# Performance work log

Hardware: AMD Instinct MI355X
Metric: run time of the kernel (lower is better)

The kernel has to match this reference:

```python
import jax, jax.numpy as jnp
import numpy as np


def _sobel_weights():
    # ImageGradientsLayer: fixed Sobel x/y filters, shape (O=2, I=1, 3, 3)
    gx = jnp.array([[-1., 0., 1.], [-2., 0., 2.], [-1., 0., 1.]], dtype=jnp.float32)
    gy = jnp.array([[-1., -2., -1.], [0., 0., 0.], [1., 2., 1.]], dtype=jnp.float32)
    return jnp.stack([gx, gy])[:, None, :, :]


def _orientation_weights():
    # SIFTOrientationLayer: 8 unit orientation vectors + 2x2 identity, shape (10, 2)
    ratios = jnp.arange(0.125, 2.125, 0.25, dtype=jnp.float32)  # 8 values
    ang = ratios * jnp.pi
    vec = jnp.stack([jnp.cos(ang), jnp.sin(ang)], axis=1)  # (8, 2)
    return jnp.concatenate([vec, jnp.eye(2, dtype=jnp.float32)], axis=0)  # (10, 2)


def setup_inputs() -> dict:
    key = jax.random.key(0)
    x = jax.random.normal(key, (8, 1, 1024, 1024), dtype=jnp.float32)
    return {"x": x, "sobel_w": _sobel_weights(), "orient_w": _orientation_weights()}


def reference(x, sobel_w, orient_w):
    # 1) ImageGradientsLayer: 3x3 Sobel conv, padding=1 -> (B, 2, H, W)
    grads = jax.lax.conv_general_dilated(
        x, sobel_w, window_strides=(1, 1), padding=((1, 1), (1, 1)),
        dimension_numbers=("NCHW", "OIHW", "NCHW"))
    # 2) SIFTOrientationLayer: 1x1 conv == channel projection -> (B, 10, H, W)
    proj = jnp.einsum("bchw,oc->bohw", grads, orient_w)
    # 3) HistogramLayer: one-hot(argmax of orientation dots) * gradient magnitude
    cosines = proj[:, :8]          # (B, 8, H, W)
    im_grads = proj[:, 8:]         # (B, 2, H, W) == grads (identity rows)
    magnitudes = jnp.sqrt(jnp.sum(im_grads * im_grads, axis=1))  # (B, H, W)
    max_idx = jnp.argmax(cosines, axis=1)                        # (B, H, W)
    onehot = jax.nn.one_hot(max_idx, 8, axis=1, dtype=x.dtype)   # (B, 8, H, W)
    hist = onehot * magnitudes[:, None, :, :]
    # 4) SubGridAccumulationLayer: depthwise 4x4 all-ones conv, pad 2 -> (B, 8, H+1, W+1)
    ones_k = jnp.ones((8, 1, 4, 4), dtype=x.dtype)
    out = jax.lax.conv_general_dilated(
        hist, ones_k, window_strides=(1, 1), padding=((2, 2), (2, 2)),
        dimension_numbers=("NCHW", "OIHW", "NCHW"), feature_group_count=8)
    return out
```

## Files before the change

kernel.cpp:

```cpp
#include <hip/hip_runtime.h>
#include <math.h>


#define WPB 4
#define TWC 61
#define WTH 16
#define BTH (WPB*WTH)
#define XC 66
#define XR (BTH+5)

__global__ __launch_bounds__(256, 4)
void sift_fused(const float* __restrict__ x,
                const float* __restrict__ ow,
                float* __restrict__ out)
{
    __shared__ float sx[XR * XC];

    const int tid  = threadIdx.x;
    const int lane = tid & 63;
    const int wv   = tid >> 6;
    const int j0 = blockIdx.x * TWC;
    const int r0 = blockIdx.y * BTH;
    const int bb = blockIdx.z;

    const float* xb = x + (size_t)bb * 1024 * 1024;
    for (int p = tid; p < XR * XC; p += 256) {
        int r = p / XC, c = p - r * XC;
        int gr = r0 - 3 + r, gc = j0 - 3 + c;
        float v = 0.0f;
        if ((unsigned)gr < 1024u && (unsigned)gc < 1024u)
            v = xb[(size_t)gr * 1024 + gc];
        sx[p] = v;
    }
    __syncthreads();

    float wcn[8], wsn[8];
    #pragma unroll
    for (int o = 0; o < 8; ++o) { wcn[o] = ow[2*o]; wsn[o] = ow[2*o+1]; }

    const int gcol = j0 - 2 + lane;
    const bool colok = (unsigned)gcol < 1024u;
    const int gj = j0 + lane;
    const bool canstore = (lane < TWC) && (gj <= 1024);
    const int rbase = r0 + WTH * wv;
    const int hbase = rbase - 2;
    const float* sxw = sx + (WTH * wv) * XC + lane;
    float* outb = out + (size_t)bb * 8u * 1025u * 1025u + gj;

    float cs0[8], cs1[8], cs2[8], cs3[8];
    #pragma unroll
    for (int o = 0; o < 8; ++o) { cs0[o]=0.f; cs1[o]=0.f; cs2[o]=0.f; cs3[o]=0.f; }

    float a0 = sxw[0],  a1 = sxw[1],    a2 = sxw[2];
    float e0 = sxw[XC], e1 = sxw[XC+1], e2 = sxw[XC+2];

#define HROW(J, D0,CT0, D1,CT1, D2,CT2, D3,CT3) { \
    float n0 = sxw[((J)+2)*XC], n1 = sxw[((J)+2)*XC+1], n2 = sxw[((J)+2)*XC+2]; \
    float gx = (a2 - a0) + 2.0f*(e2 - e0) + (n2 - n0); \
    float gy = (n0 + 2.0f*n1 + n2) - (a0 + 2.0f*a1 + a2); \
    int hrow = hbase + (J); \
    float m = (colok && (unsigned)hrow < 1024u) ? sqrtf(gx*gx + gy*gy) : 0.0f; \
    float best = gx*wcn[0] + gy*wsn[0]; int idx = 0; \
    _Pragma("unroll") \
    for (int o = 1; o < 8; ++o) { \
        float co = gx*wcn[o] + gy*wsn[o]; \
        if (co > best) { best = co; idx = o; } \
    } \
    _Pragma("unroll") \
    for (int o = 0; o < 8; ++o) { \
        float cb = (idx == o) ? m : 0.0f; \
        if (D0) CT0[o] += cb; \
        if (D1) CT1[o] += cb; \
        if (D2) CT2[o] += cb; \
        if (D3) CT3[o] += cb; \
    } \
    a0 = e0; a1 = e1; a2 = e2; e0 = n0; e1 = n1; e2 = n2; \
}

#define FIN(T, CS) { \
    int orow = rbase + (T); \
    bool ok = canstore && (orow <= 1024); \
    _Pragma("unroll") \
    for (int o = 0; o < 8; ++o) { \
        float v = CS[o]; \
        v += __shfl_down(v, 1); \
        v += __shfl_down(v, 2); \
        if (ok) outb[(size_t)o * (1025u*1025u) + (size_t)orow * 1025u] = v; \
        CS[o] = 0.0f; \
    } \
}

#define QUAD(J) \
    HROW((J),   1,cs0, 1,cs3, 1,cs2, 1,cs1) FIN((J)-3, cs1) \
    HROW((J)+1, 1,cs1, 1,cs0, 1,cs3, 1,cs2) FIN((J)-2, cs2) \
    HROW((J)+2, 1,cs2, 1,cs1, 1,cs0, 1,cs3) FIN((J)-1, cs3) \
    HROW((J)+3, 1,cs3, 1,cs2, 1,cs1, 1,cs0) FIN((J),   cs0)

    HROW(0, 1,cs0, 0,cs0, 0,cs0, 0,cs0)
    HROW(1, 1,cs1, 1,cs0, 0,cs0, 0,cs0)
    HROW(2, 1,cs2, 1,cs1, 1,cs0, 0,cs0)
    HROW(3, 1,cs3, 1,cs2, 1,cs1, 1,cs0) FIN(0, cs0)
    QUAD(4) QUAD(8) QUAD(12)
    HROW(16, 0,cs0, 1,cs3, 1,cs2, 1,cs1) FIN(13, cs1)
    HROW(17, 0,cs0, 0,cs0, 1,cs3, 1,cs2) FIN(14, cs2)
    HROW(18, 0,cs0, 0,cs0, 0,cs0, 1,cs3) FIN(15, cs3)

#undef QUAD
#undef FIN
#undef HROW
}

extern "C" void kernel_launch(void* const* d_in, const int* in_sizes, int n_in,
                              void* d_out, int out_size, void* d_ws, size_t ws_size,
                              hipStream_t stream)
{
    const float* x  = (const float*)d_in[0];
    const float* ow = (const float*)d_in[2];
    float* out = (float*)d_out;

    dim3 grid((1025 + TWC - 1) / TWC,
              (1025 + BTH - 1) / BTH,
              8);
    sift_fused<<<grid, 256, 0, stream>>>(x, ow, out);
}
```

Before: 101.8 us.

## Restructure sliding-window accumulation with pairwise partial sums and a rolled loop

The fused Sobel/orientation/histogram/box-sum kernel now keeps the vertical 4-row box sum as pairwise partial sums, (row j + row j+1) combined with an earlier pair, instead of four separate accumulators that each get eight adds per row. It also precomputes per-row horizontal Sobel differences and weighted sums once per loaded row, uses a tree-based argmax, and rolls the main row loop to shrink code size and register pressure. Warps whose rows lie entirely beyond the image exit early, and the occupancy hint is raised from 4 to 5. The risks are a changed instruction schedule from the rolled loop and possible register spills under the tighter launch bound.

```diff
diff --git a/kernel.cpp b/kernel.cpp
--- a/kernel.cpp
+++ b/kernel.cpp
@@ -2,14 +2,15 @@
 #include <math.h>
 
 
-#define WPB 4
 #define TWC 61
 #define WTH 16
+#define WPB 4
 #define BTH (WPB*WTH)
 #define XC 66
 #define XR (BTH+5)
+#define PLANE 1050625
 
-__global__ __launch_bounds__(256, 4)
+__global__ __launch_bounds__(256, 5)
 void sift_fused(const float* __restrict__ x,
                 const float* __restrict__ ow,
                 float* __restrict__ out)
@@ -34,6 +35,9 @@
     }
     __syncthreads();
 
+    const int rbase = r0 + WTH * wv;
+    if (rbase > 1024) return;
+
     float wcn[8], wsn[8];
     #pragma unroll
     for (int o = 0; o < 8; ++o) { wcn[o] = ow[2*o]; wsn[o] = ow[2*o+1]; }
@@ -42,72 +46,83 @@
     const bool colok = (unsigned)gcol < 1024u;
     const int gj = j0 + lane;
     const bool canstore = (lane < TWC) && (gj <= 1024);
-    const int rbase = r0 + WTH * wv;
-    const int hbase = rbase - 2;
-    const float* sxw = sx + (WTH * wv) * XC + lane;
-    float* outb = out + (size_t)bb * 8u * 1025u * 1025u + gj;
 
-    float cs0[8], cs1[8], cs2[8], cs3[8];
+    float* po[8];
     #pragma unroll
-    for (int o = 0; o < 8; ++o) { cs0[o]=0.f; cs1[o]=0.f; cs2[o]=0.f; cs3[o]=0.f; }
+    for (int o = 0; o < 8; ++o) po[o] = out + (size_t)(bb * 8 + o) * PLANE;
 
-    float a0 = sxw[0],  a1 = sxw[1],    a2 = sxw[2];
-    float e0 = sxw[XC], e1 = sxw[XC+1], e2 = sxw[XC+2];
+    const float* px = sx + (WTH * wv) * XC + lane;
+    int hrow = rbase - 2;
+    int orow = rbase;
+    int vo   = rbase * 1025 + gj;
 
-#define HROW(J, D0,CT0, D1,CT1, D2,CT2, D3,CT3) { \
-    float n0 = sxw[((J)+2)*XC], n1 = sxw[((J)+2)*XC+1], n2 = sxw[((J)+2)*XC+2]; \
-    float gx = (a2 - a0) + 2.0f*(e2 - e0) + (n2 - n0); \
-    float gy = (n0 + 2.0f*n1 + n2) - (a0 + 2.0f*a1 + a2); \
-    int hrow = hbase + (J); \
-    float m = (colok && (unsigned)hrow < 1024u) ? sqrtf(gx*gx + gy*gy) : 0.0f; \
-    float best = gx*wcn[0] + gy*wsn[0]; int idx = 0; \
-    _Pragma("unroll") \
-    for (int o = 1; o < 8; ++o) { \
-        float co = gx*wcn[o] + gy*wsn[o]; \
-        if (co > best) { best = co; idx = o; } \
-    } \
-    _Pragma("unroll") \
-    for (int o = 0; o < 8; ++o) { \
-        float cb = (idx == o) ? m : 0.0f; \
-        if (D0) CT0[o] += cb; \
-        if (D1) CT1[o] += cb; \
-        if (D2) CT2[o] += cb; \
-        if (D3) CT3[o] += cb; \
-    } \
-    a0 = e0; a1 = e1; a2 = e2; e0 = n0; e1 = n1; e2 = n2; \
+    float dd0, dd1, dd2, dd3, ww0, ww1, ww2, ww3;
+    float cA[8], cB[8], PP0[8], PP1[8], PP2[8], PP3[8];
+
+#define XROWLOAD(DD, WW) { \
+    float n0 = px[0], n1 = px[1], n2 = px[2]; px += XC; \
+    DD = n2 - n0; \
+    WW = n0 + 2.0f*n1 + n2; \
 }
 
-#define FIN(T, CS) { \
-    int orow = rbase + (T); \
-    bool ok = canstore && (orow <= 1024); \
+#define HSTEP(DT, DM, DB, WT, WB, CP, CC, PR, PC, DOP, DOFIN) { \
+    XROWLOAD(DB, WB) \
+    float gx = DT + 2.0f*DM + DB; \
+    float gy = WB - WT; \
+    float msq = gx*gx + gy*gy; \
+    float m = (colok && (unsigned)hrow < 1024u) \
+                ? __builtin_amdgcn_sqrtf(msq) : 0.0f; \
+    hrow++; \
+    float pj0 = gx*wcn[0] + gy*wsn[0]; \
+    float pj1 = gx*wcn[1] + gy*wsn[1]; \
+    float pj2 = gx*wcn[2] + gy*wsn[2]; \
+    float pj3 = gx*wcn[3] + gy*wsn[3]; \
+    float pj4 = gx*wcn[4] + gy*wsn[4]; \
+    float pj5 = gx*wcn[5] + gy*wsn[5]; \
+    float pj6 = gx*wcn[6] + gy*wsn[6]; \
+    float pj7 = gx*wcn[7] + gy*wsn[7]; \
+    bool g01 = pj1 > pj0; float b01 = g01 ? pj1 : pj0; int i01 = g01 ? 1 : 0; \
+    bool g23 = pj3 > pj2; float b23 = g23 ? pj3 : pj2; int i23 = g23 ? 3 : 2; \
+    bool g45 = pj5 > pj4; float b45 = g45 ? pj5 : pj4; int i45 = g45 ? 5 : 4; \
+    bool g67 = pj7 > pj6; float b67 = g67 ? pj7 : pj6; int i67 = g67 ? 7 : 6; \
+    bool gA = b23 > b01; float bA = gA ? b23 : b01; int iA = gA ? i23 : i01; \
+    bool gB = b67 > b45; float bB = gB ? b67 : b45; int iB = gB ? i67 : i45; \
+    int idx = (bB > bA) ? iB : iA; \
     _Pragma("unroll") \
-    for (int o = 0; o < 8; ++o) { \
-        float v = CS[o]; \
-        v += __shfl_down(v, 1); \
-        v += __shfl_down(v, 2); \
-        if (ok) outb[(size_t)o * (1025u*1025u) + (size_t)orow * 1025u] = v; \
-        CS[o] = 0.0f; \
+    for (int o = 0; o < 8; ++o) CC[o] = (idx == o) ? m : 0.0f; \
+    if (DOP) { \
+        _Pragma("unroll") \
+        for (int o = 0; o < 8; ++o) PC[o] = CP[o] + CC[o]; \
+    } \
+    if (DOFIN) { \
+        bool ok = canstore && (orow <= 1024); \
+        _Pragma("unroll") \
+        for (int o = 0; o < 8; ++o) { \
+            float v = PR[o] + PC[o]; \
+            v += __shfl_down(v, 1); \
+            v += __shfl_down(v, 2); \
+            if (ok) po[o][vo] = v; \
+        } \
+        vo += 1025; orow++; \
     } \
 }
 
-#define QUAD(J) \
-    HROW((J),   1,cs0, 1,cs3, 1,cs2, 1,cs1) FIN((J)-3, cs1) \
-    HROW((J)+1, 1,cs1, 1,cs0, 1,cs3, 1,cs2) FIN((J)-2, cs2) \
-    HROW((J)+2, 1,cs2, 1,cs1, 1,cs0, 1,cs3) FIN((J)-1, cs3) \
-    HROW((J)+3, 1,cs3, 1,cs2, 1,cs1, 1,cs0) FIN((J),   cs0)
+    XROWLOAD(dd0, ww0)
+    XROWLOAD(dd1, ww1)
+    HSTEP(dd0, dd1, dd2, ww0, ww2, cA, cB, PP0, PP0, 0, 0)
+    HSTEP(dd1, dd2, dd3, ww1, ww3, cB, cA, PP0, PP1, 1, 0)
+    HSTEP(dd2, dd3, dd0, ww2, ww0, cA, cB, PP0, PP2, 1, 0)
 
-    HROW(0, 1,cs0, 0,cs0, 0,cs0, 0,cs0)
-    HROW(1, 1,cs1, 1,cs0, 0,cs0, 0,cs0)
-    HROW(2, 1,cs2, 1,cs1, 1,cs0, 0,cs0)
-    HROW(3, 1,cs3, 1,cs2, 1,cs1, 1,cs0) FIN(0, cs0)
-    QUAD(4) QUAD(8) QUAD(12)
-    HROW(16, 0,cs0, 1,cs3, 1,cs2, 1,cs1) FIN(13, cs1)
-    HROW(17, 0,cs0, 0,cs0, 1,cs3, 1,cs2) FIN(14, cs2)
-    HROW(18, 0,cs0, 0,cs0, 0,cs0, 1,cs3) FIN(15, cs3)
+    #pragma unroll 1
+    for (int it = 0; it < 4; ++it) {
+        HSTEP(dd3, dd0, dd1, ww3, ww1, cB, cA, PP1, PP3, 1, 1)
+        HSTEP(dd0, dd1, dd2, ww0, ww2, cA, cB, PP2, PP0, 1, 1)
+        HSTEP(dd1, dd2, dd3, ww1, ww3, cB, cA, PP3, PP1, 1, 1)
+        HSTEP(dd2, dd3, dd0, ww2, ww0, cA, cB, PP0, PP2, 1, 1)
+    }
 
-#undef QUAD
-#undef FIN
-#undef HROW
+#undef HSTEP
+#undef XROWLOAD
 }
 
 extern "C" void kernel_launch(void* const* d_in, const int* in_sizes, int n_in,
```

Result: no change. 101.2 us (-0.6%).
